# Kernel tuning notes

Measured on AMD Instinct MI355X. Metric: run time of the kernel, lower is better.

## Reference

```python
import jax, jax.numpy as jnp
import numpy as np

N, E, F_DIM = 30000, 480000, 256
CLS_HID, NUM_CLASS, GEN_HID, MI_HID, BATCH = 128, 16, 64, 128, 4096
COM_L1, COM_L2, LAM, ALPHA, TAU, EPS = 0.5, 0.5, 0.5, 1.0, 0.5, 1e-8


def _glorot(key, shape):
    scale = jnp.sqrt(2.0 / (shape[0] + shape[-1]))
    return scale * jax.random.normal(key, shape, dtype=jnp.float32)


def setup_inputs() -> dict:
    key = jax.random.key(0)
    ks = jax.random.split(key, 32)
    inp = {
        'feat': jax.random.normal(ks[0], (N, F_DIM), dtype=jnp.float32),
        'view1_indices': jax.random.randint(ks[1], (2, E), 0, N),
        'view1_values': jax.random.uniform(ks[2], (E,), dtype=jnp.float32),
        'view2_indices': jax.random.randint(ks[3], (2, E), 0, N),
        'view2_values': jax.random.uniform(ks[4], (E,), dtype=jnp.float32),
        'idx': jnp.sort(jax.random.randint(ks[5], (BATCH,), 0, N)),
        # GenView (v1 and v2): gen_gcn weight + gen_mlp (Linear(2*gen_hid, 1))
        'W_gen_v1': _glorot(ks[6], (F_DIM, GEN_HID)),
        'Wm_v1': _glorot(ks[7], (2 * GEN_HID, 1)),
        'bm_v1': jnp.zeros((1,), dtype=jnp.float32),
        'W_gen_v2': _glorot(ks[8], (F_DIM, GEN_HID)),
        'Wm_v2': _glorot(ks[9], (2 * GEN_HID, 1)),
        'bm_v2': jnp.zeros((1,), dtype=jnp.float32),
        # Classification: three two-layer GCN encoders (v1, v2, v)
        'W1_v1': _glorot(ks[10], (F_DIM, CLS_HID)), 'W2_v1': _glorot(ks[11], (CLS_HID, NUM_CLASS)),
        'W1_v2': _glorot(ks[12], (F_DIM, CLS_HID)), 'W2_v2': _glorot(ks[13], (CLS_HID, NUM_CLASS)),
        'W1_v': _glorot(ks[14], (F_DIM, CLS_HID)), 'W2_v': _glorot(ks[15], (CLS_HID, NUM_CLASS)),
        # MI_NCE: three single GCN layers + shared projection MLP
        'Wg': _glorot(ks[16], (F_DIM, MI_HID)),
        'Wg1': _glorot(ks[17], (F_DIM, MI_HID)),
        'Wg2': _glorot(ks[18], (F_DIM, MI_HID)),
        'Wp1': _glorot(ks[19], (MI_HID, MI_HID)), 'bp1': jnp.zeros((MI_HID,), dtype=jnp.float32),
        'Wp2': _glorot(ks[20], (MI_HID, MI_HID)), 'bp2': jnp.zeros((MI_HID,), dtype=jnp.float32),
    }
    return inp


def spmm(idx, vals, x, n):
    # sparse COO adj (idx [2,E], vals [E]) @ dense x [n,d]
    return jax.ops.segment_sum(vals[:, None] * x[idx[1]], idx[0], num_segments=n)


def gcn_layer(x, idx, vals, W, n, act):
    h = spmm(idx, vals, x @ W, n)
    return jax.nn.relu(h) if act else h


def two_layer(x, idx, vals, W1, W2, n):
    return gcn_layer(gcn_layer(x, idx, vals, W1, n, True), idx, vals, W2, n, False)


def sparse_row_softmax(scores, rows, n):
    m = jax.lax.stop_gradient(jax.ops.segment_max(scores, rows, num_segments=n))
    e = jnp.exp(scores - m[rows])
    s = jax.ops.segment_sum(e, rows, num_segments=n)
    return e / s[rows]


def gen_view(feat, idx, vals, Wg, Wm, bm, com_lambda, n):
    emb = gcn_layer(feat, idx, vals, Wg, n, True)
    ff = jnp.concatenate([emb[idx[0]], emb[idx[1]]], axis=-1)  # [E, 2*gen_hid]
    temp = (ff @ Wm + bm).reshape(-1)
    pi = sparse_row_softmax(temp, idx[0], n)  # torch.sparse.softmax(dim=1)
    return vals + com_lambda * pi  # same sparsity pattern as v_ori


def sym(idx, vals):
    # normalize1 (big=True): adj + adj.T as COO concat (duplicates sum in spmm)
    return jnp.concatenate([idx, idx[::-1]], axis=1), jnp.concatenate([vals, vals])


def get_weight(prob):
    top2 = jax.lax.top_k(prob, 2)[0]
    fir, sec = top2[:, 0], top2[:, 1]
    return jnp.exp(ALPHA * (LAM * jnp.log(fir + EPS) + (1.0 - LAM) * jnp.log(fir - sec + EPS)))


def contrast_cal(z1, z2):
    num = z1 @ z2.T
    den = jnp.linalg.norm(z1, axis=-1, keepdims=True) @ jnp.linalg.norm(z2, axis=-1, keepdims=True).T
    m12 = jnp.exp(num / den / TAU)
    m21 = m12.T
    l12 = -jnp.log(jnp.diag(m12 / (m12.sum(1, keepdims=True) + EPS)) + EPS).mean()
    l21 = -jnp.log(jnp.diag(m21 / (m21.sum(1, keepdims=True) + EPS)) + EPS).mean()
    return 0.5 * (l12 + l21)


def cogsl_forward(feat, view1_values, view2_values,
                  W_gen_v1, Wm_v1, bm_v1, W_gen_v2, Wm_v2, bm_v2,
                  W1_v1, W2_v1, W1_v2, W2_v2, W1_v, W2_v,
                  Wg, Wg1, Wg2, Wp1, bp1, Wp2, bp2,
                  view1_indices, view2_indices, idx):
    n = feat.shape[0]
    # View_Estimator (GenView + normalize1)
    nv1 = gen_view(feat, view1_indices, view1_values, W_gen_v1, Wm_v1, bm_v1, COM_L1, n)
    nv2 = gen_view(feat, view2_indices, view2_values, W_gen_v2, Wm_v2, bm_v2, COM_L2, n)
    i1, v1 = sym(view1_indices, nv1)
    i2, v2 = sym(view2_indices, nv2)
    # Classification on each generated view
    prob_v1 = jax.nn.softmax(two_layer(feat, i1, v1, W1_v1, W2_v1, n), axis=1)
    prob_v2 = jax.nn.softmax(two_layer(feat, i2, v2, W1_v2, W2_v2, n), axis=1)
    logits_v1 = jnp.log(prob_v1 + EPS)
    logits_v2 = jnp.log(prob_v2 + EPS)
    # Fusion: per-node convex combination of the two sparse views (row scaling)
    w1 = get_weight(prob_v1)
    w2 = get_weight(prob_v2)
    b1 = w1 / (w1 + w2)
    b2 = w2 / (w1 + w2)
    idx_f = jnp.concatenate([i1, i2], axis=1)
    vals_f = jnp.concatenate([b1[i1[0]] * v1, b2[i2[0]] * v2])
    prob_v = jax.nn.softmax(two_layer(feat, idx_f, vals_f, W1_v, W2_v, n), axis=1)
    logits_v = jnp.log(prob_v + EPS)
    # MI_NCE over [fused v, v1, v2], big=True -> sample `batch` nodes
    proj = lambda h: jax.nn.elu(h @ Wp1 + bp1) @ Wp2 + bp2
    ev = proj(gcn_layer(feat, idx_f, vals_f, Wg, n, True))[idx]
    e1 = proj(gcn_layer(feat, i1, v1, Wg1, n, True))[idx]
    e2 = proj(gcn_layer(feat, i2, v2, Wg2, n, True))[idx]
    vv1 = contrast_cal(ev, e1)
    vv2 = contrast_cal(ev, e2)
    v1v2 = contrast_cal(e1, e2)
    return jnp.concatenate([logits_v.ravel(), logits_v1.ravel(), logits_v2.ravel(),
                            jnp.stack([vv1, vv2, v1v2])])


def reference(feat, view1_indices, view1_values, view2_indices, view2_values, idx,
              W_gen_v1, Wm_v1, bm_v1, W_gen_v2, Wm_v2, bm_v2,
              W1_v1, W2_v1, W1_v2, W2_v2, W1_v, W2_v,
              Wg, Wg1, Wg2, Wp1, bp1, Wp2, bp2):
    return cogsl_forward(feat, view1_values, view2_values,
                         W_gen_v1, Wm_v1, bm_v1, W_gen_v2, Wm_v2, bm_v2,
                         W1_v1, W2_v1, W1_v2, W2_v2, W1_v, W2_v,
                         Wg, Wg1, Wg2, Wp1, bp1, Wp2, bp2,
                         view1_indices, view2_indices, idx)
```

## Files before the change

kernel.cpp:

```cpp
#include <hip/hip_runtime.h>
#include <math.h>

#define NN 30000
#define EE 480000
#define FD 256
#define CH 128
#define NCLS 16
#define GH 64
#define MH 128
#define BT 4096
#define EPSc 1e-8f
#define GBc ((NN + 127) / 128)

typedef __attribute__((ext_vector_type(8))) short short8;
typedef __attribute__((ext_vector_type(4))) float f32x4;

__device__ __forceinline__ unsigned short f2bf(float x) {
    unsigned b = __float_as_uint(x);
    unsigned r = b + 0x7FFFu + ((b >> 16) & 1u);
    return (unsigned short)(r >> 16);
}
__device__ __forceinline__ float bf2f(unsigned short h) {
    return __uint_as_float(((unsigned)h) << 16);
}
__device__ __forceinline__ float4 fma4(float s, float4 x, float4 a) {
    a.x = fmaf(s, x.x, a.x); a.y = fmaf(s, x.y, a.y);
    a.z = fmaf(s, x.z, a.z); a.w = fmaf(s, x.w, a.w);
    return a;
}

__global__ void split_bf16(const float* __restrict__ x, unsigned short* __restrict__ hi,
                           unsigned short* __restrict__ lo, long n) {
    long i = (long)blockIdx.x * 256 + threadIdx.x;
    if (i >= n) return;
    float v = x[i];
    unsigned short h = f2bf(v);
    hi[i] = h;
    lo[i] = f2bf(v - bf2f(h));
}

struct WSArgs {
    const float* s[11];
    unsigned short* h[11];
    unsigned short* l[11];
};
__global__ void wsplit_all(WSArgs a) {
    constexpr int KK[11]  = {256,256,256,256,256,128,128,128,256,256,256};
    constexpr int NNp[11] = {64, 64, 128,128,128,16, 16, 16, 128,128,128};
    constexpr int OFF[12] = {0,16384,32768,65536,98304,131072,133120,135168,137216,169984,202752,235520};
    int i = blockIdx.x * 256 + threadIdx.x;
    if (i >= 235520) return;
    int w = 0;
#pragma unroll
    for (int t = 1; t < 11; t++) if (i >= OFF[t]) w = t;
    int j = i - OFF[w];
    int K = KK[w], N = NNp[w];
    int k = j / N, n = j % N;
    float v = a.s[w][j];
    unsigned short hh = f2bf(v);
    a.h[w][(size_t)n * K + k] = hh;
    a.l[w][(size_t)n * K + k] = f2bf(v - bf2f(hh));
}

template <int NT>
__device__ __forceinline__ void gemm3_body(
    unsigned short* sm, int bx,
    const unsigned short* __restrict__ Ahi, const unsigned short* __restrict__ Alo,
    const unsigned short* __restrict__ BThi, const unsigned short* __restrict__ BTlo,
    int K, float* __restrict__ C, int Cstride, int M)
{
    unsigned short* Ah = sm;
    unsigned short* Al = Ah + 128 * 40;
    unsigned short* Bh = Al + 128 * 40;
    unsigned short* Bl = Bh + NT * 16 * 40;
    int t = threadIdx.x;
    int w = t >> 6, l = t & 63;
    int lane = l & 15, quad = l >> 4;
    int row0 = bx * 128;
    f32x4 acc[2][NT];
#pragma unroll
    for (int s = 0; s < 2; s++)
#pragma unroll
        for (int n = 0; n < NT; n++) acc[s][n] = (f32x4)(0.f);

    int ar = t >> 1, ako = (t & 1) << 4;
    int nkc = K >> 5;
    for (int kc = 0; kc < nkc; kc++) {
        int kb = kc << 5;
        {
            int gr = row0 + ar;
            float4 h0, h1, l0, l1;
            if (gr < M) {
                const float4* pH = (const float4*)&Ahi[(size_t)gr * K + kb + ako];
                const float4* pL = (const float4*)&Alo[(size_t)gr * K + kb + ako];
                h0 = pH[0]; h1 = pH[1]; l0 = pL[0]; l1 = pL[1];
            } else {
                h0 = h1 = l0 = l1 = make_float4(0.f, 0.f, 0.f, 0.f);
            }
            float4* dH = (float4*)&Ah[ar * 40 + ako];
            dH[0] = h0; dH[1] = h1;
            float4* dL = (float4*)&Al[ar * 40 + ako];
            dL[0] = l0; dL[1] = l1;
// ... 7 lines not shown
            float4* dL = (float4*)&Bl[ar * 40 + ako];
            dL[0] = l0; dL[1] = l1;
        }
        __syncthreads();
        short8 aH[2], aL[2];
#pragma unroll
        for (int s = 0; s < 2; s++) {
            int r = w * 32 + s * 16 + lane;
            aH[s] = *(const short8*)&Ah[r * 40 + quad * 8];
            aL[s] = *(const short8*)&Al[r * 40 + quad * 8];
        }
#pragma unroll
        for (int n = 0; n < NT; n++) {
            int r = n * 16 + lane;
            short8 bH = *(const short8*)&Bh[r * 40 + quad * 8];
            short8 bL = *(const short8*)&Bl[r * 40 + quad * 8];
#pragma unroll
            for (int s = 0; s < 2; s++) {
                acc[s][n] = __builtin_amdgcn_mfma_f32_16x16x32_bf16(aH[s], bH, acc[s][n], 0, 0, 0);
                acc[s][n] = __builtin_amdgcn_mfma_f32_16x16x32_bf16(aH[s], bL, acc[s][n], 0, 0, 0);
                acc[s][n] = __builtin_amdgcn_mfma_f32_16x16x32_bf16(aL[s], bH, acc[s][n], 0, 0, 0);
            }
        }
        __syncthreads();
    }
#pragma unroll
    for (int s = 0; s < 2; s++) {
        int rb = row0 + w * 32 + s * 16 + quad * 4;
#pragma unroll
        for (int reg = 0; reg < 4; reg++) {
            int gr = rb + reg;
            if (gr >= M) continue;
#pragma unroll
            for (int n = 0; n < NT; n++)
                C[(size_t)gr * Cstride + n * 16 + lane] = acc[s][n][reg];
        }
    }
}

template <int NT, bool OUT16>
__device__ __forceinline__ void gemm1_body(
    unsigned short* sm, int bx,
    const unsigned short* __restrict__ Ahi,
    const unsigned short* __restrict__ BThi,
    int K, void* __restrict__ Cv, int Cstride, int M)
{
    unsigned short* Ah = sm;
    unsigned short* Bh = Ah + 128 * 40;
    int t = threadIdx.x;
    int w = t >> 6, l = t & 63;
    int lane = l & 15, quad = l >> 4;
    int row0 = bx * 128;
    f32x4 acc[2][NT];
#pragma unroll
    for (int s = 0; s < 2; s++)
#pragma unroll
        for (int n = 0; n < NT; n++) acc[s][n] = (f32x4)(0.f);

    int ar = t >> 1, ako = (t & 1) << 4;
    int nkc = K >> 5;
    for (int kc = 0; kc < nkc; kc++) {
        int kb = kc << 5;
        {
            int gr = row0 + ar;
            float4 h0, h1;
            if (gr < M) {
                const float4* pH = (const float4*)&Ahi[(size_t)gr * K + kb + ako];
                h0 = pH[0]; h1 = pH[1];
// ... 2 lines not shown
            }
            float4* dH = (float4*)&Ah[ar * 40 + ako];
            dH[0] = h0; dH[1] = h1;
        }
        if (ar < NT * 16) {
            const float4* pH = (const float4*)&BThi[(size_t)ar * K + kb + ako];
            float4 h0 = pH[0], h1 = pH[1];
            float4* dH = (float4*)&Bh[ar * 40 + ako];
            dH[0] = h0; dH[1] = h1;
        }
        __syncthreads();
        short8 aH[2];
#pragma unroll
        for (int s = 0; s < 2; s++)
            aH[s] = *(const short8*)&Ah[(w * 32 + s * 16 + lane) * 40 + quad * 8];
#pragma unroll
        for (int n = 0; n < NT; n++) {
            short8 bH = *(const short8*)&Bh[(n * 16 + lane) * 40 + quad * 8];
#pragma unroll
            for (int s = 0; s < 2; s++)
                acc[s][n] = __builtin_amdgcn_mfma_f32_16x16x32_bf16(aH[s], bH, acc[s][n], 0, 0, 0);
        }
        __syncthreads();
    }
#pragma unroll
    for (int s = 0; s < 2; s++) {
        int rb = row0 + w * 32 + s * 16 + quad * 4;
#pragma unroll
        for (int reg = 0; reg < 4; reg++) {
            int gr = rb + reg;
            if (gr >= M) continue;
#pragma unroll
            for (int n = 0; n < NT; n++) {
                if (OUT16) {
                    unsigned short* C = (unsigned short*)Cv;
                    C[(size_t)gr * Cstride + n * 16 + lane] = f2bf(acc[s][n][reg]);
                } else {
                    float* C = (float*)Cv;
                    C[(size_t)gr * Cstride + n * 16 + lane] = acc[s][n][reg];
                }
            }
        }
    }
}

template <int NT>
__global__ __launch_bounds__(256) void gemm3_k(
    const unsigned short* Ahi, const unsigned short* Alo, size_t yA,
    const unsigned short* BThi, const unsigned short* BTlo, size_t yB,
    int K, float* C, int Cstride, size_t yC, int M)
{
    __shared__ unsigned short sm[128 * 40 * 2 + NT * 16 * 40 * 2];
    gemm3_body<NT>(sm, blockIdx.x,
                   Ahi + blockIdx.y * yA, Alo + blockIdx.y * yA,
                   BThi + blockIdx.y * yB, BTlo + blockIdx.y * yB,
                   K, C + blockIdx.y * yC, Cstride, M);
}
template <int NT, bool OUT16>
__global__ __launch_bounds__(256) void gemm1_k(
    const unsigned short* Ahi, const unsigned short* BThi, size_t yB,
    int K, void* Cv, int Cstride, size_t yC, int M)
{
    __shared__ unsigned short sm[128 * 40 + NT * 16 * 40];
    gemm1_body<NT, OUT16>(sm, blockIdx.x, Ahi, BThi + blockIdx.y * yB, K,
                          OUT16 ? (void*)((unsigned short*)Cv + blockIdx.y * yC)
                                : (void*)((float*)Cv + blockIdx.y * yC),
                          Cstride, M);
}

__global__ __launch_bounds__(256) void mega0(
    const int* __restrict__ i1, const int* __restrict__ i2, int* __restrict__ cnt,
    int* __restrict__ sd1, int* __restrict__ sd2,
    int* __restrict__ sc1, int* __restrict__ sc2,
    const unsigned short* __restrict__ feat_hi,
    const unsigned short* __restrict__ w1vh, unsigned short* __restrict__ Ph2,
    const unsigned short* __restrict__ wgallh, unsigned short* __restrict__ Pmi16)
{
    __shared__ unsigned short sm[128 * 40 + 8 * 16 * 40];
    int b = blockIdx.x;
    if (b < GBc) {
        gemm1_body<8, true>(sm, b, feat_hi, w1vh, FD, Ph2, 128, NN);
        return;
    }
    b -= GBc;
    if (b < 3 * GBc) {
        int y = b / GBc, bx = b % GBc;
        gemm1_body<8, true>(sm, bx, feat_hi, wgallh + (size_t)y * 32768,
                            FD, Pmi16 + (size_t)y * 128, 384, NN);
        return;
    }
    b -= 3 * GBc;
    int e = b * 256 + threadIdx.x;
    if (e >= EE) return;
    int r1 = i1[e], c1 = i1[EE + e];
    int r2 = i2[e], c2 = i2[EE + e];
    sd1[e] = atomicAdd(&cnt[r1], 1);
    sd2[e] = atomicAdd(&cnt[NN + r2], 1);
    sc1[e] = atomicAdd(&cnt[2 * NN + c1], 1);
    sc2[e] = atomicAdd(&cnt[3 * NN + c2], 1);
}

__global__ __launch_bounds__(256) void mega1(
    const int* __restrict__ i1, const float* __restrict__ v1,
    const int* __restrict__ i2, const float* __restrict__ v2,
    const int* __restrict__ sd1, const int* __restrict__ sd2,
    const int* __restrict__ sc1, const int* __restrict__ sc2,
    const int* __restrict__ rp4,
    int2* __restrict__ ed1, int2* __restrict__ ec1,
    int2* __restrict__ ed2, int2* __restrict__ ec2,
    const unsigned short* __restrict__ feat_hi, const unsigned short* __restrict__ feat_lo,
    const unsigned short* __restrict__ wgen12h, const unsigned short* __restrict__ wgen12l,
    float* __restrict__ Pg,
    const unsigned short* __restrict__ w1pairh, const unsigned short* __restrict__ w1pairl,
    float* __restrict__ P01)
{
    __shared__ unsigned short sm[128 * 40 * 2 + 8 * 16 * 40 * 2];
    int b = blockIdx.x;
    if (b < GBc) {
        gemm3_body<8>(sm, b, feat_hi, feat_lo, wgen12h, wgen12l, FD, Pg, 128, NN);
        return;
    }
    b -= GBc;
    if (b < 2 * GBc) {
        int y = b / GBc, bx = b % GBc;
        gemm3_body<8>(sm, bx, feat_hi, feat_lo,
                      w1pairh + (size_t)y * 32768, w1pairl + (size_t)y * 32768,
                      FD, P01 + (size_t)y * 128, 256, NN);
        return;
    }
    b -= 2 * GBc;
    int e = b * 256 + threadIdx.x;
    if (e >= EE) return;
    const int* rp_d1 = rp4;
    const int* rp_d2 = rp4 + (NN + 1);
    const int* rp_c1 = rp4 + 2 * (NN + 1);
    const int* rp_c2 = rp4 + 3 * (NN + 1);
    int r = i1[e], c = i1[EE + e];
    int p = rp_d1[r] + sd1[e];
    ed1[p] = make_int2(c, __float_as_int(v1[e]));
    ec1[rp_c1[c] + sc1[e]] = make_int2(r, p);
    r = i2[e]; c = i2[EE + e];
    p = rp_d2[r] + sd2[e];
    ed2[p] = make_int2(c, __float_as_int(v2[e]));
    ec2[rp_c2[c] + sc2[e]] = make_int2(r, p);
}

__global__ __launch_bounds__(256) void contrast_direct(
    const unsigned short* __restrict__ z16, float* __restrict__ stats)
{
    int p = blockIdx.z;
    int pa = (p == 2) ? 1 : 0;
    int pb = (p == 0) ? 1 : 2;
    const unsigned short* A = z16 + (size_t)pa * BT * MH;
    const unsigned short* B = z16 + (size_t)pb * BT * MH;
    float* diag = stats + (size_t)p * 3 * BT;
    float* rs = diag + BT;
    float* cs = rs + BT;
    int t = threadIdx.x;
    int w = t >> 6, l = t & 63, m = l & 15, quad = l >> 4;
    int i0 = blockIdx.y * 128, j0 = blockIdx.x * 128;
// ... 152 lines not shown
    int j = p0;
    for (; j + 4 <= p1; j += 4) {
        int2 q0 = ec[j], q1 = ec[j+1], q2 = ec[j+2], q3 = ec[j+3];
        float v0 = nvd[q0.y], v1 = nvd[q1.y], v2 = nvd[q2.y], v3 = nvd[q3.y];
        a[0] = fma4(v0, x4[(size_t)q0.x * STR4 + xo], a[0]);
        a[1] = fma4(v1, x4[(size_t)q1.x * STR4 + xo], a[1]);
        a[2] = fma4(v2, x4[(size_t)q2.x * STR4 + xo], a[2]);
        a[3] = fma4(v3, x4[(size_t)q3.x * STR4 + xo], a[3]);
    }
    for (; j < p1; j++) {
        int2 q = ec[j];
        a[0] = fma4(nvd[q.y], x4[(size_t)q.x * STR4 + xo], a[0]);
    }
}

__global__ __launch_bounds__(256) void spmm64_pair(
    const int* __restrict__ rp_d, const int2* __restrict__ e1, const int2* __restrict__ e2,
    const float* __restrict__ Pg, float* __restrict__ emb)
{
    int y = blockIdx.y;
    const int* rp = rp_d + y * (NN + 1);
    const int2* arr = y ? e2 : e1;
    int row = blockIdx.x * 16 + threadIdx.x / 16;
    int o = threadIdx.x % 16;
    if (row >= NN) return;
    float4 a[4] = {};
    gath_dir_f32<32>(rp, arr, row, (const float4*)Pg, y * 16 + o, a);
    float4 r;
    r.x = fmaxf((a[0].x + a[1].x) + (a[2].x + a[3].x), 0.f);
    r.y = fmaxf((a[0].y + a[1].y) + (a[2].y + a[3].y), 0.f);
    r.z = fmaxf((a[0].z + a[1].z) + (a[2].z + a[3].z), 0.f);
    r.w = fmaxf((a[0].w + a[1].w) + (a[2].w + a[3].w), 0.f);
    ((float4*)emb)[((size_t)y * NN + row) * 16 + o] = r;
}

__global__ __launch_bounds__(256) void spmm128_pair(
    const int* __restrict__ rp_d, const int* __restrict__ rp_c,
    const int2* __restrict__ ed1, const int2* __restrict__ ec1, const float* __restrict__ nvd1,
    const int2* __restrict__ ed2, const int2* __restrict__ ec2, const float* __restrict__ nvd2,
    const float* __restrict__ P01, float* __restrict__ Q01)
{
    int y = blockIdx.y;
    const int* rpd = rp_d + y * (NN + 1);
    const int* rpc = rp_c + y * (NN + 1);
    const int2* ed = y ? ed2 : ed1;
    const int2* ec = y ? ec2 : ec1;
    const float* nvd = y ? nvd2 : nvd1;
    int row = blockIdx.x * 8 + threadIdx.x / 32;
    int o = threadIdx.x % 32;
    if (row >= NN) return;
    int xo = y * 32 + o;
    float4 a[4] = {};
    gath_dir_f32<64>(rpd, ed, row, (const float4*)P01, xo, a);
    gath_csc_f32<64>(rpc, ec, nvd, row, (const float4*)P01, xo, a);
    float4 r;
    r.x = fmaxf((a[0].x + a[1].x) + (a[2].x + a[3].x), 0.f);
    r.y = fmaxf((a[0].y + a[1].y) + (a[2].y + a[3].y), 0.f);
    r.z = fmaxf((a[0].z + a[1].z) + (a[2].z + a[3].z), 0.f);
    r.w = fmaxf((a[0].w + a[1].w) + (a[2].w + a[3].w), 0.f);
    ((float4*)Q01)[((size_t)y * NN + row) * 32 + o] = r;
}

__global__ __launch_bounds__(256) void spmm16_pair(
    const int* __restrict__ rp_d, const int* __restrict__ rp_c,
    const int2* __restrict__ ed1, const int2* __restrict__ ec1, const float* __restrict__ nvd1,
    const int2* __restrict__ ed2, const int2* __restrict__ ec2, const float* __restrict__ nvd2,
    const float* __restrict__ R01, float* __restrict__ T01)
{
    int y = blockIdx.y;
    const int* rpd = rp_d + y * (NN + 1);
    const int* rpc = rp_c + y * (NN + 1);
    const int2* ed = y ? ed2 : ed1;
    const int2* ec = y ? ec2 : ec1;
    const float* nvd = y ? nvd2 : nvd1;
    int row = blockIdx.x * 64 + threadIdx.x / 4;
    int o = threadIdx.x % 4;
    if (row >= NN) return;
    const float4* x4 = (const float4*)(R01 + (size_t)y * NN * 16);
    float4 a[4] = {};
    gath_dir_f32<4>(rpd, ed, row, x4, o, a);
    gath_csc_f32<4>(rpc, ec, nvd, row, x4, o, a);
    float4 r;
    r.x = (a[0].x + a[1].x) + (a[2].x + a[3].x);
    r.y = (a[0].y + a[1].y) + (a[2].y + a[3].y);
    r.z = (a[0].z + a[1].z) + (a[2].z + a[3].z);
    r.w = (a[0].w + a[1].w) + (a[2].w + a[3].w);
    ((float4*)(T01 + (size_t)y * NN * 16))[(size_t)row * 4 + o] = r;
}

__global__ __launch_bounds__(256) void spmm16_fused(
    const int* __restrict__ rp_d, const int* __restrict__ rp_c,
    const int2* __restrict__ ed1, const int2* __restrict__ ec1, const float* __restrict__ nvd1,
    const int2* __restrict__ ed2, const int2* __restrict__ ec2, const float* __restrict__ nvd2,
// ... 60 lines not shown
    }
}
__device__ __forceinline__ void gath_csc_b16(
    const int* __restrict__ rp, const int2* __restrict__ ec, const float* __restrict__ nvd,
    int row, const unsigned short* __restrict__ X, int xstride, int o, float* acc)
{
    int p0 = rp[row], p1 = rp[row + 1];
    int j = p0;
    for (; j + 4 <= p1; j += 4) {
        int2 q0 = ec[j], q1 = ec[j+1], q2 = ec[j+2], q3 = ec[j+3];
        short8 x0 = *(const short8*)&X[(size_t)q0.x * xstride + o * 8];
        short8 x1 = *(const short8*)&X[(size_t)q1.x * xstride + o * 8];
        short8 x2 = *(const short8*)&X[(size_t)q2.x * xstride + o * 8];
        short8 x3 = *(const short8*)&X[(size_t)q3.x * xstride + o * 8];
        float v0 = nvd[q0.y], v1 = nvd[q1.y], v2 = nvd[q2.y], v3 = nvd[q3.y];
#pragma unroll
        for (int k = 0; k < 8; k++) {
            acc[k] = fmaf(v0, bf2f((unsigned short)x0[k]), acc[k]);
            acc[k] = fmaf(v1, bf2f((unsigned short)x1[k]), acc[k]);
            acc[k] = fmaf(v2, bf2f((unsigned short)x2[k]), acc[k]);
            acc[k] = fmaf(v3, bf2f((unsigned short)x3[k]), acc[k]);
        }
    }
    for (; j < p1; j++) {
        int2 q = ec[j];
        short8 xv = *(const short8*)&X[(size_t)q.x * xstride + o * 8];
        float v = nvd[q.y];
#pragma unroll
        for (int k = 0; k < 8; k++)
            acc[k] = fmaf(v, bf2f((unsigned short)xv[k]), acc[k]);
    }
}

__global__ __launch_bounds__(256) void fused128_b16(
    const int* __restrict__ rp_d, const int* __restrict__ rp_c,
    const int2* __restrict__ ed1, const int2* __restrict__ ec1, const float* __restrict__ nvd1,
    const int2* __restrict__ ed2, const int2* __restrict__ ec2, const float* __restrict__ nvd2,
    const float* __restrict__ bb, const unsigned short* __restrict__ X,
    unsigned short* __restrict__ Out)
{
    int row = blockIdx.x * 16 + threadIdx.x / 16;
    int o = threadIdx.x % 16;
    if (row >= NN) return;
    float a1[8] = {}, a2[8] = {};
    gath_dir_b16(rp_d, ed1, row, X, 128, o, a1);
    gath_csc_b16(rp_c, ec1, nvd1, row, X, 128, o, a1);
    gath_dir_b16(rp_d + (NN + 1), ed2, row, X, 128, o, a2);
    gath_csc_b16(rp_c + (NN + 1), ec2, nvd2, row, X, 128, o, a2);
    float w1 = bb[row], w2 = bb[NN + row];
    short8 outv;
#pragma unroll
    for (int k = 0; k < 8; k++) {
        float r = fmaxf(w1 * a1[k] + w2 * a2[k], 0.f);
        outv[k] = (short)f2bf(r);
    }
    *(short8*)&Out[(size_t)row * 128 + o * 8] = outv;
}

__global__ __launch_bounds__(256) void rows_spmm_b16(
    const int* __restrict__ rp_d, const int* __restrict__ rp_c,
    const int2* __restrict__ ed1, const int2* __restrict__ ec1, const float* __restrict__ nvd1,
    const int2* __restrict__ ed2, const int2* __restrict__ ec2, const float* __restrict__ nvd2,
    const float* __restrict__ bb, const int* __restrict__ rows,
    const unsigned short* __restrict__ Pmi, float* __restrict__ zQ)
{
    int y = blockIdx.y;
    int ri = blockIdx.x * 16 + threadIdx.x / 16;
    int o = threadIdx.x % 16;
    if (ri >= BT) return;
    int node = rows[ri];
    int xoff = (y == 0) ? 0 : ((y == 1) ? 128 : 256);
    const unsigned short* X = Pmi + xoff;
    float acc[8] = {};
    if (y == 0) {
        float a1[8] = {}, a2[8] = {};
        gath_dir_b16(rp_d, ed1, node, X, 384, o, a1);
        gath_csc_b16(rp_c, ec1, nvd1, node, X, 384, o, a1);
        gath_dir_b16(rp_d + (NN + 1), ed2, node, X, 384, o, a2);
        gath_csc_b16(rp_c + (NN + 1), ec2, nvd2, node, X, 384, o, a2);
        float w1 = bb[node], w2 = bb[NN + node];
#pragma unroll
        for (int k = 0; k < 8; k++) acc[k] = w1 * a1[k] + w2 * a2[k];
    } else if (y == 1) {
        gath_dir_b16(rp_d, ed1, node, X, 384, o, acc);
        gath_csc_b16(rp_c, ec1, nvd1, node, X, 384, o, acc);
    } else {
        gath_dir_b16(rp_d + (NN + 1), ed2, node, X, 384, o, acc);
        gath_csc_b16(rp_c + (NN + 1), ec2, nvd2, node, X, 384, o, acc);
    }
    float* out = zQ + ((size_t)y * BT + ri) * 128 + o * 8;
#pragma unroll
    for (int k = 0; k < 8; k++) out[k] = fmaxf(acc[k], 0.f);
}

__global__ __launch_bounds__(256) void node_scores_pair(
    const float* __restrict__ emb, const float* __restrict__ Wm1,
    const float* __restrict__ Wm2, float* __restrict__ sb)
{
    int y = blockIdx.y;
    const float* e_ = emb + (size_t)y * NN * GH;
    const float* Wm = y ? Wm2 : Wm1;
    int node = blockIdx.x * 4 + threadIdx.x / 64;
    int lane = threadIdx.x % 64;
    if (node >= NN) return;
    float e = e_[(size_t)node * GH + lane];
    float vb = e * Wm[GH + lane];
#pragma unroll
    for (int off = 32; off; off >>= 1)
        vb += __shfl_down(vb, off);
    if (lane == 0) sb[y * NN + node] = vb;
}

__global__ void softmax16y(const float* __restrict__ S01, float* __restrict__ logits_base,
                           float* __restrict__ w12)
{
    int y = blockIdx.y;
    const float* S = S01 + (size_t)y * NN * NCLS;
    float* logits = logits_base + (size_t)y * NN * NCLS;
    float* w = w12 + (size_t)y * NN;
    int node = blockIdx.x * 256 + threadIdx.x;
    if (node >= NN) return;
    float v[NCLS];
    float mx = -3.4e38f;
#pragma unroll
    for (int j = 0; j < NCLS; j++) { v[j] = S[(size_t)node * NCLS + j]; mx = fmaxf(mx, v[j]); }
    float s = 0.f;
#pragma unroll
// ... 70 lines not shown
    const float* diag = stats + (size_t)p * 3 * BT;
    const float* rs = diag + BT;
    const float* cs = rs + BT;
    float s1 = 0.f, s2 = 0.f;
    for (int i = t; i < BT; i += 256) {
        float d = diag[i];
        s1 += logf(d / (rs[i] + EPSc) + EPSc);
        s2 += logf(d / (cs[i] + EPSc) + EPSc);
    }
#pragma unroll
    for (int off = 32; off; off >>= 1) { s1 += __shfl_down(s1, off); s2 += __shfl_down(s2, off); }
    __shared__ float sh[8];
    if ((t & 63) == 0) { sh[(t >> 6) * 2] = s1; sh[(t >> 6) * 2 + 1] = s2; }
    __syncthreads();
    if (t == 0) {
        float a = sh[0] + sh[2] + sh[4] + sh[6];
        float b = sh[1] + sh[3] + sh[5] + sh[7];
        out3[p] = 0.5f * (-a / BT - b / BT);
    }
}

extern "C" void kernel_launch(void* const* d_in, const int* in_sizes, int n_in,
                              void* d_out, int out_size, void* d_ws, size_t ws_size,
                              hipStream_t stream)
{
    const float* feat   = (const float*)d_in[0];
    const int*   ind1   = (const int*)d_in[1];
    const float* vals1  = (const float*)d_in[2];
    const int*   ind2   = (const int*)d_in[3];
    const float* vals2  = (const float*)d_in[4];
    const int*   idxb   = (const int*)d_in[5];
    const float* Wm1    = (const float*)d_in[7];
    const float* Wm2    = (const float*)d_in[10];
    const float* Wp1    = (const float*)d_in[21];
    const float* bp1    = (const float*)d_in[22];
    const float* Wp2    = (const float*)d_in[23];
    const float* bp2    = (const float*)d_in[24];
    float* dout = (float*)d_out;

    float* ws = (float*)d_ws;
    size_t off = 0;
    auto alloc = [&](size_t n) { n = (n + 3) & ~(size_t)3; float* p = ws + off; off += n; return p; };
    auto alloc_s = [&](size_t n) { return (unsigned short*)alloc((n + 1) / 2); };

    float* pool = alloc(24960000);
    float* Pg   = pool;
    float* P01  = pool + 3840000;
    float* emb  = pool + 11520000;
    float* Q01  = pool + 11520000;
    unsigned short* q01h = (unsigned short*)pool;
    unsigned short* q01l = (unsigned short*)(pool + 19200000);
    float* R01  = pool + 23040000;
    float* T01  = pool + 24000000;
    unsigned short* q2h = (unsigned short*)pool;
    float* R2   = pool + 960000;
    float* T2   = pool + 1440000;
    float* zQ   = pool + 1920000;

    unsigned short* feat_hi = alloc_s((size_t)NN * FD);
    unsigned short* feat_lo = alloc_s((size_t)NN * FD);
    unsigned short* Ph2d    = alloc_s((size_t)NN * CH);
    unsigned short* Pmi16d  = alloc_s((size_t)NN * 384);
    float* sb   = alloc(2 * NN);
    float* w12  = alloc(2 * NN);
    float* bb   = alloc(2 * NN);
    float* stats = alloc((size_t)3 * 3 * BT);
    unsigned short* z16 = alloc_s((size_t)3 * BT * MH);
    int2* ed1 = (int2*)alloc(2 * (size_t)EE);
    int2* ed2 = (int2*)alloc(2 * (size_t)EE);
    int2* ec1 = (int2*)alloc(2 * (size_t)EE);
    int2* ec2 = (int2*)alloc(2 * (size_t)EE);
    float* nvd1 = alloc(EE);
    float* nvd2 = alloc(EE);
    int* sd1 = (int*)alloc(EE);
    int* sd2 = (int*)alloc(EE);
    int* sc1 = (int*)alloc(EE);
    int* sc2 = (int*)alloc(EE);
    int* rp4  = (int*)alloc(4 * (NN + 1));
    int* cnt4 = (int*)alloc(4 * NN);
    int* bsum = (int*)alloc(128);
    int* rp_d = rp4;
    int* rp_c = rp4 + 2 * (NN + 1);
    unsigned short* wgen12h = alloc_s(32768); unsigned short* wgen12l = alloc_s(32768);
    unsigned short* w1pairh = alloc_s(65536); unsigned short* w1pairl = alloc_s(65536);
    unsigned short* w1vh    = alloc_s(32768); unsigned short* w1vl    = alloc_s(32768);
    unsigned short* w2pairh = alloc_s(4096);  unsigned short* w2pairl = alloc_s(4096);
    unsigned short* w2vh    = alloc_s(2048);  unsigned short* w2vl    = alloc_s(2048);
    unsigned short* wgallh  = alloc_s(98304); unsigned short* wgalll  = alloc_s(98304);

    const int NB = (NN + 1 + 1023) / 1024;
    const int NCNT = (EE + 255) / 256;

    hipMemsetAsync(cnt4, 0, 4 * NN * 4, stream);
    split_bf16<<<((long)NN * FD + 255) / 256, 256, 0, stream>>>(feat, feat_hi, feat_lo, (long)NN * FD);
    {
        WSArgs a;
        a.s[0] = (const float*)d_in[6];  a.h[0] = wgen12h;          a.l[0] = wgen12l;
        a.s[1] = (const float*)d_in[9];  a.h[1] = wgen12h + 16384;  a.l[1] = wgen12l + 16384;
        a.s[2] = (const float*)d_in[12]; a.h[2] = w1pairh;          a.l[2] = w1pairl;
        a.s[3] = (const float*)d_in[14]; a.h[3] = w1pairh + 32768;  a.l[3] = w1pairl + 32768;
        a.s[4] = (const float*)d_in[16]; a.h[4] = w1vh;             a.l[4] = w1vl;
        a.s[5] = (const float*)d_in[13]; a.h[5] = w2pairh;          a.l[5] = w2pairl;
        a.s[6] = (const float*)d_in[15]; a.h[6] = w2pairh + 2048;   a.l[6] = w2pairl + 2048;
        a.s[7] = (const float*)d_in[17]; a.h[7] = w2vh;             a.l[7] = w2vl;
        a.s[8] = (const float*)d_in[18]; a.h[8] = wgallh;           a.l[8] = wgalll;
        a.s[9] = (const float*)d_in[19]; a.h[9] = wgallh + 32768;   a.l[9] = wgalll + 32768;
        a.s[10]= (const float*)d_in[20]; a.h[10]= wgallh + 65536;   a.l[10]= wgalll + 65536;
        wsplit_all<<<(235520 + 255) / 256, 256, 0, stream>>>(a);
    }

    mega0<<<4 * GBc + NCNT, 256, 0, stream>>>(ind1, ind2, cnt4, sd1, sd2, sc1, sc2,
                                              feat_hi, w1vh, Ph2d, wgallh, Pmi16d);

    scan_block4<<<dim3(NB, 4), 1024, 0, stream>>>(cnt4, rp4, bsum);
    scan_bsum4<<<4, 64, 0, stream>>>(bsum, NB);
    scan_add4<<<dim3(NB, 4), 1024, 0, stream>>>(bsum, rp4);

    mega1<<<3 * GBc + NCNT, 256, 0, stream>>>(ind1, vals1, ind2, vals2,
                                              sd1, sd2, sc1, sc2, rp4,
                                              ed1, ec1, ed2, ec2,
                                              feat_hi, feat_lo, wgen12h, wgen12l, Pg,
                                              w1pairh, w1pairl, P01);

    spmm64_pair<<<dim3((NN + 15) / 16, 2), 256, 0, stream>>>(rp_d, ed1, ed2, Pg, emb);
    node_scores_pair<<<dim3((NN + 3) / 4, 2), 256, 0, stream>>>(emb, Wm1, Wm2, sb);
    gen_nv<<<dim3((NN + 255) / 256, 2), 256, 0, stream>>>(rp_d, ed1, ed2, sb, nvd1, nvd2);

    spmm128_pair<<<dim3((NN + 7) / 8, 2), 256, 0, stream>>>(rp_d, rp_c, ed1, ec1, nvd1,
                                                            ed2, ec2, nvd2, P01, Q01);
    split_bf16<<<((long)2 * NN * CH + 255) / 256, 256, 0, stream>>>(Q01, q01h, q01l, (long)2 * NN * CH);
    gemm3_k<1><<<dim3(GBc, 2), 256, 0, stream>>>(q01h, q01l, (size_t)NN * CH,
                                                 w2pairh, w2pairl, 2048,
                                                 CH, R01, 16, (size_t)NN * NCLS, NN);
    spmm16_pair<<<dim3((NN + 63) / 64, 2), 256, 0, stream>>>(rp_d, rp_c, ed1, ec1, nvd1,
                                                             ed2, ec2, nvd2, R01, T01);
    softmax16y<<<dim3((NN + 255) / 256, 2), 256, 0, stream>>>(T01, dout + (size_t)NN * NCLS, w12);
    bweights<<<(NN + 255) / 256, 256, 0, stream>>>(w12, bb);

    fused128_b16<<<(NN + 15) / 16, 256, 0, stream>>>(rp_d, rp_c, ed1, ec1, nvd1,
                                                     ed2, ec2, nvd2, bb, Ph2d, q2h);
    gemm1_k<1, false><<<dim3(GBc, 1), 256, 0, stream>>>(q2h, w2vh, 0, CH, R2, 16, 0, NN);
    spmm16_fused<<<(NN + 63) / 64, 256, 0, stream>>>(rp_d, rp_c, ed1, ec1, nvd1,
                                                     ed2, ec2, nvd2, bb, R2, T2);
    softmax16<<<(NN + 255) / 256, 256, 0, stream>>>(T2, dout);

    rows_spmm_b16<<<dim3((BT + 15) / 16, 3), 256, 0, stream>>>(rp_d, rp_c, ed1, ec1, nvd1,
                                                               ed2, ec2, nvd2, bb, idxb, Pmi16d, zQ);
    proj_norm3<<<dim3(BT, 3), 128, 0, stream>>>(zQ, Wp1, bp1, Wp2, bp2, z16);

    hipMemsetAsync(stats, 0, (size_t)3 * 3 * BT * 4, stream);
    contrast_direct<<<dim3(32, 32, 3), 256, 0, stream>>>(z16, stats);
    contrast_reduce<<<3, 256, 0, stream>>>(stats, dout + (size_t)3 * NN * NCLS);
}
```

Measured before the change: 872.6 us.

## Fuse 128-wide SpMM with small W2 projection and co-schedule MI row gathers

The second-layer aggregation for the two views is now fused with the 128x16 W2 multiply, done in fp32 from shared memory. This replaces the former sequence of a 128-wide SpMM, a bf16 split pass and a 3-pass MFMA GEMM, so the large Q intermediates are no longer written to and re-read from global memory. The fused-view path does the same thing in place of fused128_b16 plus gemm1_k. The MI batch-row gathers are split across two new merged kernels (mega2, mega3), so they share launches with the SpMM work and the standalone rows kernel is dropped. In exchange the small GEMM runs on scalar FMAs using only half the threads in mega2, and each block now has a shared-memory staging step plus a barrier.

Result: faster. 821.9 us (-5.8%).

```diff
diff --git a/kernel.cpp b/kernel.cpp
--- a/kernel.cpp
+++ b/kernel.cpp
@@ -11,6 +11,9 @@
 #define BT 4096
 #define EPSc 1e-8f
 #define GBc ((NN + 127) / 128)
+#define SPB8 ((NN + 7) / 8)
+#define SPB16 ((NN + 15) / 16)
+#define RBc ((BT + 15) / 16)
 
 typedef __attribute__((ext_vector_type(8))) short short8;
 typedef __attribute__((ext_vector_type(4))) float f32x4;
@@ -40,34 +43,33 @@
 }
 
 struct WSArgs {
-    const float* s[11];
-    unsigned short* h[11];
-    unsigned short* l[11];
+    const float* s[8];
+    unsigned short* h[8];
+    unsigned short* l[8];
 };
 __global__ void wsplit_all(WSArgs a) {
-    constexpr int KK[11]  = {256,256,256,256,256,128,128,128,256,256,256};
-    constexpr int NNp[11] = {64, 64, 128,128,128,16, 16, 16, 128,128,128};
-    constexpr int OFF[12] = {0,16384,32768,65536,98304,131072,133120,135168,137216,169984,202752,235520};
+    constexpr int NNp[8] = {64, 64, 128, 128, 128, 128, 128, 128};
+    constexpr int OFF[9] = {0, 16384, 32768, 65536, 98304, 131072, 163840, 196608, 229376};
     int i = blockIdx.x * 256 + threadIdx.x;
-    if (i >= 235520) return;
+    if (i >= 229376) return;
     int w = 0;
 #pragma unroll
-    for (int t = 1; t < 11; t++) if (i >= OFF[t]) w = t;
+    for (int t = 1; t < 8; t++) if (i >= OFF[t]) w = t;
     int j = i - OFF[w];
-    int K = KK[w], N = NNp[w];
+    int N = NNp[w];
     int k = j / N, n = j % N;
     float v = a.s[w][j];
     unsigned short hh = f2bf(v);
-    a.h[w][(size_t)n * K + k] = hh;
-    a.l[w][(size_t)n * K + k] = f2bf(v - bf2f(hh));
-}
-
-template <int NT>
+    a.h[w][(size_t)n * 256 + k] = hh;
+    a.l[w][(size_t)n * 256 + k] = f2bf(v - bf2f(hh));
+}
+
+template <int NT, bool OUT16>
 __device__ __forceinline__ void gemm3_body(
     unsigned short* sm, int bx,
     const unsigned short* __restrict__ Ahi, const unsigned short* __restrict__ Alo,
     const unsigned short* __restrict__ BThi, const unsigned short* __restrict__ BTlo,
-    int K, float* __restrict__ C, int Cstride, int M)
+    int K, void* __restrict__ Cv, int Cstride, int M)
 {
     unsigned short* Ah = sm;
     unsigned short* Al = Ah + 128 * 40;
@@ -141,8 +143,12 @@
             int gr = rb + reg;
             if (gr >= M) continue;
 #pragma unroll
-            for (int n = 0; n < NT; n++)
-                C[(size_t)gr * Cstride + n * 16 + lane] = acc[s][n][reg];
+            for (int n = 0; n < NT; n++) {
+                if (OUT16)
+                    ((unsigned short*)Cv)[(size_t)gr * Cstride + n * 16 + lane] = f2bf(acc[s][n][reg]);
+                else
+                    ((float*)Cv)[(size_t)gr * Cstride + n * 16 + lane] = acc[s][n][reg];
+            }
         }
     }
 }
@@ -211,40 +217,13 @@
             if (gr >= M) continue;
 #pragma unroll
             for (int n = 0; n < NT; n++) {
-                if (OUT16) {
-                    unsigned short* C = (unsigned short*)Cv;
-                    C[(size_t)gr * Cstride + n * 16 + lane] = f2bf(acc[s][n][reg]);
-                } else {
-                    float* C = (float*)Cv;
-                    C[(size_t)gr * Cstride + n * 16 + lane] = acc[s][n][reg];
-                }
+                if (OUT16)
+                    ((unsigned short*)Cv)[(size_t)gr * Cstride + n * 16 + lane] = f2bf(acc[s][n][reg]);
+                else
+                    ((float*)Cv)[(size_t)gr * Cstride + n * 16 + lane] = acc[s][n][reg];
             }
         }
     }
-}
-
-template <int NT>
-__global__ __launch_bounds__(256) void gemm3_k(
-    const unsigned short* Ahi, const unsigned short* Alo, size_t yA,
-    const unsigned short* BThi, const unsigned short* BTlo, size_t yB,
-    int K, float* C, int Cstride, size_t yC, int M)
-{
-    __shared__ unsigned short sm[128 * 40 * 2 + NT * 16 * 40 * 2];
-    gemm3_body<NT>(sm, blockIdx.x,
-                   Ahi + blockIdx.y * yA, Alo + blockIdx.y * yA,
-                   BThi + blockIdx.y * yB, BTlo + blockIdx.y * yB,
-                   K, C + blockIdx.y * yC, Cstride, M);
-}
-template <int NT, bool OUT16>
-__global__ __launch_bounds__(256) void gemm1_k(
-    const unsigned short* Ahi, const unsigned short* BThi, size_t yB,
-    int K, void* Cv, int Cstride, size_t yC, int M)
-{
-    __shared__ unsigned short sm[128 * 40 + NT * 16 * 40];
-    gemm1_body<NT, OUT16>(sm, blockIdx.x, Ahi, BThi + blockIdx.y * yB, K,
-                          OUT16 ? (void*)((unsigned short*)Cv + blockIdx.y * yC)
-                                : (void*)((float*)Cv + blockIdx.y * yC),
-                          Cstride, M);
 }
 
 __global__ __launch_bounds__(256) void mega0(
@@ -296,15 +275,15 @@
     __shared__ unsigned short sm[128 * 40 * 2 + 8 * 16 * 40 * 2];
     int b = blockIdx.x;
     if (b < GBc) {
-        gemm3_body<8>(sm, b, feat_hi, feat_lo, wgen12h, wgen12l, FD, Pg, 128, NN);
+        gemm3_body<8, false>(sm, b, feat_hi, feat_lo, wgen12h, wgen12l, FD, Pg, 128, NN);
         return;
     }
     b -= GBc;
     if (b < 2 * GBc) {
         int y = b / GBc, bx = b % GBc;
-        gemm3_body<8>(sm, bx, feat_hi, feat_lo,
-                      w1pairh + (size_t)y * 32768, w1pairl + (size_t)y * 32768,
-                      FD, P01 + (size_t)y * 128, 256, NN);
+        gemm3_body<8, false>(sm, bx, feat_hi, feat_lo,
+                             w1pairh + (size_t)y * 32768, w1pairl + (size_t)y * 32768,
+                             FD, P01 + (size_t)y * 128, 256, NN);
         return;
     }
     b -= 2 * GBc;
@@ -523,33 +502,6 @@
     r.z = fmaxf((a[0].z + a[1].z) + (a[2].z + a[3].z), 0.f);
     r.w = fmaxf((a[0].w + a[1].w) + (a[2].w + a[3].w), 0.f);
     ((float4*)emb)[((size_t)y * NN + row) * 16 + o] = r;
-}
-
-__global__ __launch_bounds__(256) void spmm128_pair(
-    const int* __restrict__ rp_d, const int* __restrict__ rp_c,
-    const int2* __restrict__ ed1, const int2* __restrict__ ec1, const float* __restrict__ nvd1,
-    const int2* __restrict__ ed2, const int2* __restrict__ ec2, const float* __restrict__ nvd2,
-    const float* __restrict__ P01, float* __restrict__ Q01)
-{
-    int y = blockIdx.y;
-    const int* rpd = rp_d + y * (NN + 1);
-    const int* rpc = rp_c + y * (NN + 1);
-    const int2* ed = y ? ed2 : ed1;
-    const int2* ec = y ? ec2 : ec1;
-    const float* nvd = y ? nvd2 : nvd1;
-    int row = blockIdx.x * 8 + threadIdx.x / 32;
-    int o = threadIdx.x % 32;
-    if (row >= NN) return;
-    int xo = y * 32 + o;
-    float4 a[4] = {};
-    gath_dir_f32<64>(rpd, ed, row, (const float4*)P01, xo, a);
-    gath_csc_f32<64>(rpc, ec, nvd, row, (const float4*)P01, xo, a);
-    float4 r;
-    r.x = fmaxf((a[0].x + a[1].x) + (a[2].x + a[3].x), 0.f);
-    r.y = fmaxf((a[0].y + a[1].y) + (a[2].y + a[3].y), 0.f);
-    r.z = fmaxf((a[0].z + a[1].z) + (a[2].z + a[3].z), 0.f);
-    r.w = fmaxf((a[0].w + a[1].w) + (a[2].w + a[3].w), 0.f);
-    ((float4*)Q01)[((size_t)y * NN + row) * 32 + o] = r;
 }
 
 __global__ __launch_bounds__(256) void spmm16_pair(
@@ -676,40 +628,14 @@
     }
 }
 
-__global__ __launch_bounds__(256) void fused128_b16(
-    const int* __restrict__ rp_d, const int* __restrict__ rp_c,
-    const int2* __restrict__ ed1, const int2* __restrict__ ec1, const float* __restrict__ nvd1,
-    const int2* __restrict__ ed2, const int2* __restrict__ ec2, const float* __restrict__ nvd2,
-    const float* __restrict__ bb, const unsigned short* __restrict__ X,
-    unsigned short* __restrict__ Out)
-{
-    int row = blockIdx.x * 16 + threadIdx.x / 16;
-    int o = threadIdx.x % 16;
-    if (row >= NN) return;
-    float a1[8] = {}, a2[8] = {};
-    gath_dir_b16(rp_d, ed1, row, X, 128, o, a1);
-    gath_csc_b16(rp_c, ec1, nvd1, row, X, 128, o, a1);
-    gath_dir_b16(rp_d + (NN + 1), ed2, row, X, 128, o, a2);
-    gath_csc_b16(rp_c + (NN + 1), ec2, nvd2, row, X, 128, o, a2);
-    float w1 = bb[row], w2 = bb[NN + row];
-    short8 outv;
-#pragma unroll
-    for (int k = 0; k < 8; k++) {
-        float r = fmaxf(w1 * a1[k] + w2 * a2[k], 0.f);
-        outv[k] = (short)f2bf(r);
-    }
-    *(short8*)&Out[(size_t)row * 128 + o * 8] = outv;
-}
-
-__global__ __launch_bounds__(256) void rows_spmm_b16(
-    const int* __restrict__ rp_d, const int* __restrict__ rp_c,
+__device__ __forceinline__ void rows_b16_body(
+    int bx, int y, const int* __restrict__ rp_d, const int* __restrict__ rp_c,
     const int2* __restrict__ ed1, const int2* __restrict__ ec1, const float* __restrict__ nvd1,
     const int2* __restrict__ ed2, const int2* __restrict__ ec2, const float* __restrict__ nvd2,
     const float* __restrict__ bb, const int* __restrict__ rows,
     const unsigned short* __restrict__ Pmi, float* __restrict__ zQ)
 {
-    int y = blockIdx.y;
-    int ri = blockIdx.x * 16 + threadIdx.x / 16;
+    int ri = bx * 16 + threadIdx.x / 16;
     int o = threadIdx.x % 16;
     if (ri >= BT) return;
     int node = rows[ri];
@@ -737,6 +663,126 @@
     for (int k = 0; k < 8; k++) out[k] = fmaxf(acc[k], 0.f);
 }
 
+__device__ __forceinline__ void spmm128f_body(
+    float* sm, int bx, int y, const int* __restrict__ rp_d, const int* __restrict__ rp_c,
+    const int2* __restrict__ ed, const int2* __restrict__ ec, const float* __restrict__ nvd,
+    const float* __restrict__ P01, const float* __restrict__ W2, float* __restrict__ R01)
+{
+    float* W2s = sm;
+    float* Qs  = sm + 2048;
+    for (int i = threadIdx.x; i < 2048; i += 256) W2s[i] = W2[i];
+    int r = threadIdx.x / 32;
+    int o = threadIdx.x % 32;
+    int row = bx * 8 + r;
+    float4 a[4] = {};
+    if (row < NN) {
+        gath_dir_f32<64>(rp_d + y * (NN + 1), ed, row, (const float4*)P01, y * 32 + o, a);
+        gath_csc_f32<64>(rp_c + y * (NN + 1), ec, nvd, row, (const float4*)P01, y * 32 + o, a);
+    }
+    float4 q;
+    q.x = fmaxf((a[0].x + a[1].x) + (a[2].x + a[3].x), 0.f);
+    q.y = fmaxf((a[0].y + a[1].y) + (a[2].y + a[3].y), 0.f);
+    q.z = fmaxf((a[0].z + a[1].z) + (a[2].z + a[3].z), 0.f);
+    q.w = fmaxf((a[0].w + a[1].w) + (a[2].w + a[3].w), 0.f);
+    *(float4*)&Qs[r * 128 + o * 4] = q;
+    __syncthreads();
+    int t = threadIdx.x;
+    if (t < 128) {
+        int rr = t >> 4, c = t & 15;
+        int grow = bx * 8 + rr;
+        if (grow < NN) {
+            float acc = 0.f;
+            const float* qrow = &Qs[rr * 128];
+#pragma unroll 8
+            for (int k = 0; k < 128; k++)
+                acc = fmaf(qrow[k], W2s[k * 16 + c], acc);
+            R01[((size_t)y * NN + grow) * 16 + c] = acc;
+        }
+    }
+}
+
+__device__ __forceinline__ void fused128b2_body(
+    float* sm, int bx, const int* __restrict__ rp_d, const int* __restrict__ rp_c,
+    const int2* __restrict__ ed1, const int2* __restrict__ ec1, const float* __restrict__ nvd1,
+    const int2* __restrict__ ed2, const int2* __restrict__ ec2, const float* __restrict__ nvd2,
+    const float* __restrict__ bb, const unsigned short* __restrict__ Ph2,
+    const float* __restrict__ W2v, float* __restrict__ R2)
+{
+    float* W2s = sm;
+    float* Qs  = sm + 2048;
+    for (int i = threadIdx.x; i < 2048; i += 256) W2s[i] = W2v[i];
+    int r = threadIdx.x / 16;
+    int o = threadIdx.x % 16;
+    int row = bx * 16 + r;
+    float a1[8] = {}, a2[8] = {};
+    float w1 = 0.f, w2 = 0.f;
+    if (row < NN) {
+        gath_dir_b16(rp_d, ed1, row, Ph2, 128, o, a1);
+        gath_csc_b16(rp_c, ec1, nvd1, row, Ph2, 128, o, a1);
+        gath_dir_b16(rp_d + (NN + 1), ed2, row, Ph2, 128, o, a2);
+        gath_csc_b16(rp_c + (NN + 1), ec2, nvd2, row, Ph2, 128, o, a2);
+        w1 = bb[row]; w2 = bb[NN + row];
+    }
+#pragma unroll
+    for (int k = 0; k < 8; k++)
+        Qs[r * 128 + o * 8 + k] = fmaxf(w1 * a1[k] + w2 * a2[k], 0.f);
+    __syncthreads();
+    int t = threadIdx.x;
+    int rr = t >> 4, c = t & 15;
+    int grow = bx * 16 + rr;
+    if (grow < NN) {
+        float acc = 0.f;
+        const float* qrow = &Qs[rr * 128];
+#pragma unroll 8
+        for (int k = 0; k < 128; k++)
+            acc = fmaf(qrow[k], W2s[k * 16 + c], acc);
+        R2[(size_t)grow * 16 + c] = acc;
+    }
+}
+
+__global__ __launch_bounds__(256) void mega2(
+    const int* __restrict__ rp_d, const int* __restrict__ rp_c,
+    const int2* __restrict__ ed1, const int2* __restrict__ ec1, const float* __restrict__ nvd1,
+    const int2* __restrict__ ed2, const int2* __restrict__ ec2, const float* __restrict__ nvd2,
+    const float* __restrict__ P01, const float* __restrict__ W2v1, const float* __restrict__ W2v2,
+    float* __restrict__ R01,
+    const int* __restrict__ rows, const unsigned short* __restrict__ Pmi,
+    float* __restrict__ zQ)
+{
+    __shared__ float sm[2048 + 8 * 128];
+    int b = blockIdx.x;
+    if (b < 2 * SPB8) {
+        int y = b / SPB8;
+        spmm128f_body(sm, b % SPB8, y, rp_d, rp_c, y ? ed2 : ed1, y ? ec2 : ec1,
+                      y ? nvd2 : nvd1, P01, y ? W2v2 : W2v1, R01);
+        return;
+    }
+    b -= 2 * SPB8;
+    int y = 1 + b / RBc;
+    rows_b16_body(b % RBc, y, rp_d, rp_c, ed1, ec1, nvd1, ed2, ec2, nvd2,
+                  nullptr, rows, Pmi, zQ);
+}
+
+__global__ __launch_bounds__(256) void mega3(
+    const int* __restrict__ rp_d, const int* __restrict__ rp_c,
+    const int2* __restrict__ ed1, const int2* __restrict__ ec1, const float* __restrict__ nvd1,
+    const int2* __restrict__ ed2, const int2* __restrict__ ec2, const float* __restrict__ nvd2,
+    const float* __restrict__ bb, const unsigned short* __restrict__ Ph2,
+    const float* __restrict__ W2v, float* __restrict__ R2,
+    const int* __restrict__ rows, const unsigned short* __restrict__ Pmi,
+    float* __restrict__ zQ)
+{
+    __shared__ float sm[2048 + 16 * 128];
+    int b = blockIdx.x;
+    if (b < SPB16) {
+        fused128b2_body(sm, b, rp_d, rp_c, ed1, ec1, nvd1, ed2, ec2, nvd2,
+                        bb, Ph2, W2v, R2);
+        return;
+    }
+    rows_b16_body(b - SPB16, 0, rp_d, rp_c, ed1, ec1, nvd1, ed2, ec2, nvd2,
+                  bb, rows, Pmi, zQ);
+}
+
 __global__ __launch_bounds__(256) void node_scores_pair(
     const float* __restrict__ emb, const float* __restrict__ Wm1,
     const float* __restrict__ Wm2, float* __restrict__ sb)
@@ -873,6 +919,9 @@
     const int*   idxb   = (const int*)d_in[5];
     const float* Wm1    = (const float*)d_in[7];
     const float* Wm2    = (const float*)d_in[10];
+    const float* W2_v1  = (const float*)d_in[13];
+    const float* W2_v2  = (const float*)d_in[15];
+    const float* W2_v   = (const float*)d_in[17];
     const float* Wp1    = (const float*)d_in[21];
     const float* bp1    = (const float*)d_in[22];
     const float* Wp2    = (const float*)d_in[23];
@@ -888,15 +937,11 @@
     float* Pg   = pool;
     float* P01  = pool + 3840000;
     float* emb  = pool + 11520000;
-    float* Q01  = pool + 11520000;
-    unsigned short* q01h = (unsigned short*)pool;
-    unsigned short* q01l = (unsigned short*)(pool + 19200000);
-    float* R01  = pool + 23040000;
-    float* T01  = pool + 24000000;
-    unsigned short* q2h = (unsigned short*)pool;
-    float* R2   = pool + 960000;
-    float* T2   = pool + 1440000;
-    float* zQ   = pool + 1920000;
+    float* R01  = pool + 15360000;
+    float* T01  = pool + 16400000;
+    float* zQ   = pool + 17400000;
+    float* R2   = pool;
+    float* T2   = pool + 500000;
 
     unsigned short* feat_hi = alloc_s((size_t)NN * FD);
     unsigned short* feat_lo = alloc_s((size_t)NN * FD);
@@ -925,8 +970,6 @@
     unsigned short* wgen12h = alloc_s(32768); unsigned short* wgen12l = alloc_s(32768);
     unsigned short* w1pairh = alloc_s(65536); unsigned short* w1pairl = alloc_s(65536);
     unsigned short* w1vh    = alloc_s(32768); unsigned short* w1vl    = alloc_s(32768);
-    unsigned short* w2pairh = alloc_s(4096);  unsigned short* w2pairl = alloc_s(4096);
-    unsigned short* w2vh    = alloc_s(2048);  unsigned short* w2vl    = alloc_s(2048);
     unsigned short* wgallh  = alloc_s(98304); unsigned short* wgalll  = alloc_s(98304);
 
     const int NB = (NN + 1 + 1023) / 1024;
@@ -941,13 +984,10 @@
         a.s[2] = (const float*)d_in[12]; a.h[2] = w1pairh;          a.l[2] = w1pairl;
         a.s[3] = (const float*)d_in[14]; a.h[3] = w1pairh + 32768;  a.l[3] = w1pairl + 32768;
         a.s[4] = (const float*)d_in[16]; a.h[4] = w1vh;             a.l[4] = w1vl;
-        a.s[5] = (const float*)d_in[13]; a.h[5] = w2pairh;          a.l[5] = w2pairl;
-        a.s[6] = (const float*)d_in[15]; a.h[6] = w2pairh + 2048;   a.l[6] = w2pairl + 2048;
-        a.s[7] = (const float*)d_in[17]; a.h[7] = w2vh;             a.l[7] = w2vl;
-        a.s[8] = (const float*)d_in[18]; a.h[8] = wgallh;           a.l[8] = wgalll;
-        a.s[9] = (const float*)d_in[19]; a.h[9] = wgallh + 32768;   a.l[9] = wgalll + 32768;
-        a.s[10]= (const float*)d_in[20]; a.h[10]= wgallh + 65536;   a.l[10]= wgalll + 65536;
-        wsplit_all<<<(235520 + 255) / 256, 256, 0, stream>>>(a);
+        a.s[5] = (const float*)d_in[18]; a.h[5] = wgallh;           a.l[5] = wgalll;
+        a.s[6] = (const float*)d_in[19]; a.h[6] = wgallh + 32768;   a.l[6] = wgalll + 32768;
+        a.s[7] = (const float*)d_in[20]; a.h[7] = wgallh + 65536;   a.l[7] = wgalll + 65536;
+        wsplit_all<<<(229376 + 255) / 256, 256, 0, stream>>>(a);
     }
 
     mega0<<<4 * GBc + NCNT, 256, 0, stream>>>(ind1, ind2, cnt4, sd1, sd2, sc1, sc2,
@@ -967,28 +1007,23 @@
     node_scores_pair<<<dim3((NN + 3) / 4, 2), 256, 0, stream>>>(emb, Wm1, Wm2, sb);
     gen_nv<<<dim3((NN + 255) / 256, 2), 256, 0, stream>>>(rp_d, ed1, ed2, sb, nvd1, nvd2);
 
-    spmm128_pair<<<dim3((NN + 7) / 8, 2), 256, 0, stream>>>(rp_d, rp_c, ed1, ec1, nvd1,
-                                                            ed2, ec2, nvd2, P01, Q01);
-    split_bf16<<<((long)2 * NN * CH + 255) / 256, 256, 0, stream>>>(Q01, q01h, q01l, (long)2 * NN * CH);
-    gemm3_k<1><<<dim3(GBc, 2), 256, 0, stream>>>(q01h, q01l, (size_t)NN * CH,
-                                                 w2pairh, w2pairl, 2048,
-                                                 CH, R01, 16, (size_t)NN * NCLS, NN);
+    mega2<<<2 * SPB8 + 2 * RBc, 256, 0, stream>>>(rp_d, rp_c, ed1, ec1, nvd1,
+                                                  ed2, ec2, nvd2, P01, W2_v1, W2_v2,
+                                                  R01, idxb, Pmi16d, zQ);
+
     spmm16_pair<<<dim3((NN + 63) / 64, 2), 256, 0, stream>>>(rp_d, rp_c, ed1, ec1, nvd1,
                                                              ed2, ec2, nvd2, R01, T01);
     softmax16y<<<dim3((NN + 255) / 256, 2), 256, 0, stream>>>(T01, dout + (size_t)NN * NCLS, w12);
     bweights<<<(NN + 255) / 256, 256, 0, stream>>>(w12, bb);
 
-    fused128_b16<<<(NN + 15) / 16, 256, 0, stream>>>(rp_d, rp_c, ed1, ec1, nvd1,
-                                                     ed2, ec2, nvd2, bb, Ph2d, q2h);
-    gemm1_k<1, false><<<dim3(GBc, 1), 256, 0, stream>>>(q2h, w2vh, 0, CH, R2, 16, 0, NN);
+    mega3<<<SPB16 + RBc, 256, 0, stream>>>(rp_d, rp_c, ed1, ec1, nvd1, ed2, ec2, nvd2,
+                                           bb, Ph2d, W2_v, R2, idxb, Pmi16d, zQ);
+
     spmm16_fused<<<(NN + 63) / 64, 256, 0, stream>>>(rp_d, rp_c, ed1, ec1, nvd1,
                                                      ed2, ec2, nvd2, bb, R2, T2);
     softmax16<<<(NN + 255) / 256, 256, 0, stream>>>(T2, dout);
 
-    rows_spmm_b16<<<dim3((BT + 15) / 16, 3), 256, 0, stream>>>(rp_d, rp_c, ed1, ec1, nvd1,
-                                                               ed2, ec2, nvd2, bb, idxb, Pmi16d, zQ);
     proj_norm3<<<dim3(BT, 3), 128, 0, stream>>>(zQ, Wp1, bp1, Wp2, bp2, z16);
-
     hipMemsetAsync(stats, 0, (size_t)3 * 3 * BT * 4, stream);
     contrast_direct<<<dim3(32, 32, 3), 256, 0, stream>>>(z16, stats);
     contrast_reduce<<<3, 256, 0, stream>>>(stats, dout + (size_t)3 * NN * NCLS);
```
